# Performance work log

Hardware: AMD Instinct MI355X
Metric: run time of the kernel (lower is better)

The kernel has to match this reference:

```python
import jax, jax.numpy as jnp
import numpy as np
from jax import lax

C = 128
N_HEADS = 4
HEAD_D = C // N_HEADS
EXP = 2  # FFN expansion


def _ln_c(x, g, b, eps):
    # LayerNorm over channel dim of NCHW (equivalent to to_3d -> LN(c) -> to_4d)
    m = jnp.mean(x, axis=1, keepdims=True)
    v = jnp.mean((x - m) ** 2, axis=1, keepdims=True)
    return (x - m) / jnp.sqrt(v + eps) * g[None, :, None, None] + b[None, :, None, None]


def _conv1x1(x, w, b):
    # w: (out, in)
    return jnp.einsum('bchw,oc->bohw', x, w) + b[None, :, None, None]


def _dwconv(x, w, b):
    # depthwise conv, w: (Cg, 1, k, k), stride 1, SAME padding
    y = lax.conv_general_dilated(
        x, w, window_strides=(1, 1), padding='SAME',
        dimension_numbers=('NCHW', 'OIHW', 'NCHW'),
        feature_group_count=x.shape[1])
    return y + b[None, :, None, None]


def setup_inputs() -> dict:
    key = jax.random.key(0)
    ks = jax.random.split(key, 24)
    s = 0.05
    hid = C
    e = EXP * C
    inp = {
        'feats1': jax.random.normal(ks[0], (2, C, 64, 256), jnp.float32),
        'feats2': jax.random.normal(ks[1], (2, C, 64, 256), jnp.float32),
        # attention norms
        'an_g': jnp.ones((C,), jnp.float32), 'an_b': jnp.zeros((C,), jnp.float32),
        'anc_g': jnp.ones((C,), jnp.float32), 'anc_b': jnp.zeros((C,), jnp.float32),
        # qkv / out 1x1 convs
        'wq': jax.random.normal(ks[2], (hid, C), jnp.float32) * s,
        'bq': jnp.zeros((hid,), jnp.float32),
        'wkv': jax.random.normal(ks[3], (2 * hid, C), jnp.float32) * s,
        'bkv': jnp.zeros((2 * hid,), jnp.float32),
        'wo': jax.random.normal(ks[4], (C, hid), jnp.float32) * s,
        'bo': jnp.zeros((C,), jnp.float32),
        # FFN
        'fn_g': jnp.ones((C,), jnp.float32), 'fn_b': jnp.zeros((C,), jnp.float32),
        'w_in': jax.random.normal(ks[5], (e, C), jnp.float32) * s,
        'b_in': jnp.zeros((e,), jnp.float32),
        'w_dw3': jax.random.normal(ks[6], (e, 1, 3, 3), jnp.float32) * s,
        'b_dw3': jnp.zeros((e,), jnp.float32),
        'w_dw5': jax.random.normal(ks[7], (e, 1, 5, 5), jnp.float32) * s,
        'b_dw5': jnp.zeros((e,), jnp.float32),
        'w_dw7': jax.random.normal(ks[8], (e, 1, 7, 7), jnp.float32) * s,
        'b_dw7': jnp.zeros((e,), jnp.float32),
        'w_pw': jax.random.normal(ks[9], (e, 3 * e), jnp.float32) * s,
        'b_pw': jnp.zeros((e,), jnp.float32),
        'w_out': jax.random.normal(ks[10], (C, e), jnp.float32) * s,
        'b_out': jnp.zeros((C,), jnp.float32),
    }
    return inp


def reference(feats1, feats2, an_g, an_b, anc_g, anc_b, wq, bq, wkv, bkv, wo, bo,
              fn_g, fn_b, w_in, b_in, w_dw3, b_dw3, w_dw5, b_dw5, w_dw7, b_dw7,
              w_pw, b_pw, w_out, b_out):
    eps = 1e-6
    hid = C
    n, d = N_HEADS, HEAD_D
    scale = d ** (-0.5)

    # bi-directional cross attention: doubled batch
    cat1 = jnp.concatenate([feats1, feats2], axis=0)  # (B, C, H, W)
    cat2 = jnp.concatenate([feats2, feats1], axis=0)
    B, _, H, W = cat1.shape

    # pre-norm (separate norms for query and context streams)
    x1 = _ln_c(cat1, an_g, an_b, eps)
    x2 = _ln_c(cat2, anc_g, anc_b, eps)

    q = _conv1x1(x1, wq, bq)                     # (B, hid, H, W)
    kv = _conv1x1(x2, wkv, bkv)
    k, v = kv[:, :hid], kv[:, hid:]

    qh = q.reshape(B, n, d, H, W)
    kh = k.reshape(B, n, d, H, W)
    vh = v.reshape(B, n, d, H, W)

    # per-row (epipolar) attention over width
    sim = jnp.einsum('bndhi,bndhj->bnhij', qh, kh) * scale  # (B, n, H, W, W)
    # sink competition renorm
    attn = jax.nn.softmax(sim, axis=-1) + eps
    attn = attn / jnp.sum(attn, axis=-1, keepdims=True)

    o = jnp.einsum('bnhij,bndhj->bndhi', attn, vh).reshape(B, hid, H, W)
    o = _conv1x1(o, wo, bo)
    cat1 = cat1 + o

    # multiscale depthwise-conv FFN (receptive_aug='conv')
    y = _ln_c(cat1, fn_g, fn_b, 1e-5)
    y = jax.nn.silu(_conv1x1(y, w_in, b_in))     # (B, 2C, H, W)
    f3 = _dwconv(y, w_dw3, b_dw3)
    f5 = _dwconv(y, w_dw5, b_dw5)
    f7 = _dwconv(y, w_dw7, b_dw7)
    y = y + jax.nn.silu(_conv1x1(jnp.concatenate([f3, f5, f7], axis=1), w_pw, b_pw))
    y = _conv1x1(y, w_out, b_out)
    cat1 = cat1 + y

    half = B // 2
    return cat1[:half], cat1[half:]
```

## Files before the change

kernel.cpp:

```cpp
#include <hip/hip_runtime.h>

typedef unsigned short u16;
typedef unsigned int u32;

constexpr int H_ = 64;
constexpr int W_ = 256;
constexpr int HW_ = H_ * W_;

typedef __bf16 bf16x8 __attribute__((ext_vector_type(8)));
typedef float f32x4 __attribute__((ext_vector_type(4)));

__device__ __forceinline__ float bf2f(u16 v) { return __uint_as_float(((u32)v) << 16); }
__device__ __forceinline__ u16 f2bf(float f) {
  u32 x = __float_as_uint(f);
  u32 r = (x + 0x7fffu + ((x >> 16) & 1u)) >> 16;
  return (u16)r;
}
__device__ __forceinline__ float lo2f(u32 p) { return __uint_as_float(p << 16); }
__device__ __forceinline__ float hi2f(u32 p) { return __uint_as_float(p & 0xffff0000u); }
__device__ __forceinline__ void unpack8(uint4 v, float* f) {
  f[0] = lo2f(v.x); f[1] = hi2f(v.x);
  f[2] = lo2f(v.y); f[3] = hi2f(v.y);
  f[4] = lo2f(v.z); f[5] = hi2f(v.z);
  f[6] = lo2f(v.w); f[7] = hi2f(v.w);
}
__device__ __forceinline__ bf16x8 as_bf16x8(uint4 v) {
  union { uint4 u; bf16x8 b; } x; x.u = v; return x.b;
}
__device__ __forceinline__ int swz(int p, int c) { return c ^ (((p >> 3) & 3) << 3); }

constexpr int NT = 26;
constexpr int ELEMS_PER_BLK = 4096;
struct CvtArgs {
  const void* src[NT];
  u32 dst_off[NT];
  u32 n[NT];
  u32 blk_start[NT];
};

__global__ void convert_all(CvtArgs a, u16* __restrict__ dst) {
  const u32 bid = blockIdx.x;
  int ti = 0;
#pragma unroll
  for (int k = 1; k < NT; ++k) if (a.blk_start[k] <= bid) ti = k;
  const u32 e0 = (bid - a.blk_start[ti]) * ELEMS_PER_BLK;
  const u32 n = a.n[ti];
  u32 hi = e0 + ELEMS_PER_BLK; if (hi > n) hi = n;
  const float* sp = (const float*)a.src[ti];
  u16* d = dst + a.dst_off[ti];
  for (u32 i = e0 + threadIdx.x; i < hi; i += 256) d[i] = f2bf(sp[i]);
}

template <int CIN, int COUT>
__launch_bounds__(256)
__global__ void gemm1x1_ln(const u16* __restrict__ xA, const u16* __restrict__ xB,
                           const u16* __restrict__ w, const u16* __restrict__ bias,
                           const u16* __restrict__ lng, const u16* __restrict__ lnb,
                           float lneps, u16* __restrict__ out) {
  constexpr int POS = 64;
  constexpr int PITCH = CIN + 8;
  constexpr int MT = COUT / 64;
  __shared__ __align__(16) u16 xs[POS * PITCH];
  __shared__ float red1[256], red2[256], stm[64], str[64];
  const int t = threadIdx.x;
  const int b = blockIdx.y;
  const int pos0 = blockIdx.x * POS;

  const u16* basep = (b >= 2) ? xB : xA;
  const int bb = (b < 2) ? b : b - 2;
  const u16* xb16 = basep + (size_t)bb * CIN * HW_;

  constexpr int NLOAD = CIN * POS / 8;
  for (int idx = t; idx < NLOAD; idx += 256) {
    const int c = idx / (POS / 8);
    const int p8 = (idx % (POS / 8)) * 8;
    uint4 v = *(const uint4*)(xb16 + (size_t)c * HW_ + pos0 + p8);
    const int csw = swz(p8, c);
    u16* row = xs + p8 * PITCH + csw;
    row[0]         = (u16)v.x; row[PITCH]     = (u16)(v.x >> 16);
    row[2 * PITCH] = (u16)v.y; row[3 * PITCH] = (u16)(v.y >> 16);
    row[4 * PITCH] = (u16)v.z; row[5 * PITCH] = (u16)(v.z >> 16);
    row[6 * PITCH] = (u16)v.w; row[7 * PITCH] = (u16)(v.w >> 16);
  }
  __syncthreads();

  {
    const int p = t & 63, part = t >> 6;
    const int xorp = ((p >> 3) & 3) << 3;
    float s = 0.f, sq = 0.f;
#pragma unroll
    for (int k = 0; k < 32; k += 8) {
      uint4 v = *(const uint4*)(xs + p * PITCH + ((part * 32 + k) ^ xorp));
      float f[8]; unpack8(v, f);
#pragma unroll
      for (int j = 0; j < 8; ++j) { s += f[j]; sq += f[j] * f[j]; }
    }
    red1[part * 64 + p] = s; red2[part * 64 + p] = sq;
    __syncthreads();
    if (t < 64) {
      float ss = red1[t] + red1[64 + t] + red1[128 + t] + red1[192 + t];
      float qq = red2[t] + red2[64 + t] + red2[128 + t] + red2[192 + t];
      float m = ss * (1.0f / CIN);
      float var = qq * (1.0f / CIN) - m * m;
      var = var < 0.f ? 0.f : var;
      stm[t] = m; str[t] = rsqrtf(var + lneps);
    }
    __syncthreads();
    const float m = stm[p], r = str[p];
#pragma unroll
    for (int k = 0; k < 32; k += 8) {
      const int c = part * 32 + k;
      uint4 v = *(const uint4*)(xs + p * PITCH + (c ^ xorp));
      float f[8]; unpack8(v, f);
      u32 pk[4];
#pragma unroll
      for (int j = 0; j < 8; j += 2) {
        float g0 = bf2f(lng[c + j]), be0 = bf2f(lnb[c + j]);
        float g1 = bf2f(lng[c + j + 1]), be1 = bf2f(lnb[c + j + 1]);
        u16 lo = f2bf((f[j] - m) * r * g0 + be0);
        u16 hi = f2bf((f[j + 1] - m) * r * g1 + be1);
        pk[j >> 1] = (u32)lo | ((u32)hi << 16);
      }
      uint4 ov; ov.x = pk[0]; ov.y = pk[1]; ov.z = pk[2]; ov.w = pk[3];
      *(uint4*)(xs + p * PITCH + (c ^ xorp)) = ov;
    }
    __syncthreads();
  }

  const int lane = t & 63, wv = t >> 6;
  const int lo16 = lane & 15, quad = lane >> 4;
  const int orow0 = wv * MT * 16;
  const int qrow = quad * 4;

  f32x4 acc[MT][4];
#pragma unroll
  for (int mt = 0; mt < MT; ++mt) {
#pragma unroll
    for (int r = 0; r < 4; ++r) {
      const float bv = bf2f(bias[orow0 + mt * 16 + qrow + r]);
#pragma unroll
      for (int nt = 0; nt < 4; ++nt) acc[mt][nt][r] = bv;
    }
  }

  const u16* xb[4];
#pragma unroll
  for (int nt = 0; nt < 4; ++nt) {
    const int row = nt * 16 + lo16;
    xb[nt] = xs + row * PITCH + (quad * 8 ^ ((((row >> 3) & 3)) << 3));
  }
  const u16* wl = w + (size_t)(orow0 + lo16) * CIN + quad * 8;

#pragma unroll 2
  for (int kc = 0; kc < CIN / 32; ++kc) {
    const int c0 = kc * 32;
    bf16x8 bfr[4];
#pragma unroll
    for (int nt = 0; nt < 4; ++nt)
      bfr[nt] = as_bf16x8(*(const uint4*)(xb[nt] + c0));
#pragma unroll
    for (int mt = 0; mt < MT; ++mt) {
      bf16x8 afr = as_bf16x8(*(const uint4*)(wl + (size_t)mt * 16 * CIN + c0));
#pragma unroll
      for (int nt = 0; nt < 4; ++nt)
        acc[mt][nt] = __builtin_amdgcn_mfma_f32_16x16x32_bf16(afr, bfr[nt], acc[mt][nt], 0, 0, 0);
    }
  }

#pragma unroll
  for (int mt = 0; mt < MT; ++mt) {
#pragma unroll
    for (int nt = 0; nt < 4; ++nt) {
#pragma unroll
      for (int r = 0; r < 4; ++r) {
        const int o = orow0 + mt * 16 + qrow + r;
        const int p = pos0 + nt * 16 + lo16;
        out[((size_t)b * COUT + o) * HW_ + p] = f2bf(acc[mt][nt][r]);
      }
    }
  }
}

__launch_bounds__(256)
__global__ void attn_mfma(const u16* __restrict__ qb, const u16* __restrict__ kvb,
                          u16* __restrict__ ob) {
  constexpr int PA = 40;
  constexpr int PJ = 264;
  __shared__ __align__(16) u16 kT[256 * PA];
  __shared__ __align__(16) u16 vT[32 * PJ];
  __shared__ __align__(16) u16 PlO[4 * 16 * PJ];
  const int t = threadIdx.x;
  const int h = blockIdx.x, n = blockIdx.y, b = blockIdx.z;
  const size_t qbase = ((size_t)(b * 128 + n * 32)) * HW_ + (size_t)h * W_;
  const size_t kbase = ((size_t)(b * 256 + n * 32)) * HW_ + (size_t)h * W_;
  const size_t vbase = ((size_t)(b * 256 + 128 + n * 32)) * HW_ + (size_t)h * W_;

#pragma unroll
  for (int d8 = 0; d8 < 4; ++d8) {
    u32 pk[4];
#pragma unroll
    for (int j = 0; j < 4; ++j) {
      u32 lo = kvb[kbase + (size_t)(d8 * 8 + 2 * j) * HW_ + t];
      u32 hi = kvb[kbase + (size_t)(d8 * 8 + 2 * j + 1) * HW_ + t];
      pk[j] = lo | (hi << 16);
    }
    *(uint4*)(kT + t * PA + d8 * 8) = make_uint4(pk[0], pk[1], pk[2], pk[3]);
  }
#pragma unroll
  for (int k = 0; k < 16; ++k) {
    const int idx = k * 256 + t;
    const int d = idx >> 7, p2 = (idx & 127) * 2;
    u32 v = *(const u32*)(kvb + vbase + (size_t)d * HW_ + p2);
    *(u32*)(vT + d * PJ + p2) = v;
  }
  __syncthreads();

  const int lane = t & 63, wv = t >> 6;
  const int lo16 = lane & 15, quad = lane >> 4;
  const float scale = 0.17677669529663687f;
  const float renorm = 1.0f / (1.0f + 256.0f * 1e-6f);
  const float addc = 1e-6f * renorm;
  u16* Pw = PlO + wv * 16 * PJ;

  f32x4 oacc[4][2];
  for (int ii = 0; ii < 4; ++ii) {
    const int i0 = ii * 64 + wv * 16;
    u16 qr[8];
#pragma unroll
    for (int j = 0; j < 8; ++j)
      qr[j] = qb[qbase + (size_t)(quad * 8 + j) * HW_ + i0 + lo16];
    bf16x8 qa;
#pragma unroll
    for (int j = 0; j < 8; ++j) qa[j] = *(__bf16*)&qr[j];
    f32x4 s[16];
#pragma unroll
    for (int jt = 0; jt < 16; ++jt) {
      bf16x8 kb = as_bf16x8(*(const uint4*)(kT + (jt * 16 + lo16) * PA + quad * 8));
      f32x4 z = {0.f, 0.f, 0.f, 0.f};
      s[jt] = __builtin_amdgcn_mfma_f32_16x16x32_bf16(qa, kb, z, 0, 0, 0);
    }
#pragma unroll
    for (int r = 0; r < 4; ++r) {
      float sum = 0.f;
#pragma unroll
      for (int jt = 0; jt < 16; ++jt) {
        float e = __expf(s[jt][r] * scale);
        s[jt][r] = e; sum += e;
      }
#pragma unroll
      for (int off = 1; off <= 8; off <<= 1) sum += __shfl_xor(sum, off, 64);
      const float inv2 = renorm / sum;
#pragma unroll
      for (int jt = 0; jt < 16; ++jt)
        Pw[(quad * 4 + r) * PJ + jt * 16 + lo16] = f2bf(fmaf(s[jt][r], inv2, addc));
    }
    f32x4 o0 = {0.f, 0.f, 0.f, 0.f}, o1 = {0.f, 0.f, 0.f, 0.f};
#pragma unroll
    for (int kt = 0; kt < 8; ++kt) {
      bf16x8 pa = as_bf16x8(*(const uint4*)(Pw + lo16 * PJ + kt * 32 + quad * 8));
      bf16x8 v0 = as_bf16x8(*(const uint4*)(vT + lo16 * PJ + kt * 32 + quad * 8));
      bf16x8 v1 = as_bf16x8(*(const uint4*)(vT + (16 + lo16) * PJ + kt * 32 + quad * 8));
      o0 = __builtin_amdgcn_mfma_f32_16x16x32_bf16(pa, v0, o0, 0, 0, 0);
      o1 = __builtin_amdgcn_mfma_f32_16x16x32_bf16(pa, v1, o1, 0, 0, 0);
    }
    oacc[ii][0] = o0; oacc[ii][1] = o1;
  }
  __syncthreads();
  u16* Ob = PlO;
#pragma unroll
  for (int ii = 0; ii < 4; ++ii) {
    const int i0 = ii * 64 + wv * 16;
#pragma unroll
    for (int r = 0; r < 4; ++r) {
      Ob[(i0 + quad * 4 + r) * PA + lo16] = f2bf(oacc[ii][0][r]);
      Ob[(i0 + quad * 4 + r) * PA + 16 + lo16] = f2bf(oacc[ii][1][r]);
    }
  }
  __syncthreads();
  for (int d = 0; d < 32; ++d) ob[qbase + (size_t)d * HW_ + t] = Ob[t * PA + d];
}

__launch_bounds__(256)
__global__ void fused_proj_ffn(const u16* __restrict__ obf,
                               const u16* __restrict__ wo, const u16* __restrict__ bo_,
                               const float* __restrict__ f1, const float* __restrict__ f2,
                               const u16* __restrict__ fng, const u16* __restrict__ fnb,
                               const u16* __restrict__ w_in, const u16* __restrict__ b_in,
                               u16* __restrict__ cat1b, u16* __restrict__ yb) {
  constexpr int PITCH = 136;
  __shared__ __align__(16) u16 xs[64 * PITCH];
  __shared__ float red1[256], red2[256], stm[64], str[64];
  const int t = threadIdx.x;
  const int b = blockIdx.y;
  const int pos0 = blockIdx.x * 64;
  const u16* xb16 = obf + (size_t)b * 128 * HW_;

  for (int idx = t; idx < 1024; idx += 256) {
    const int c = idx >> 3, p8 = (idx & 7) * 8;
    uint4 v = *(const uint4*)(xb16 + (size_t)c * HW_ + pos0 + p8);
    const int csw = swz(p8, c);
    u16* row = xs + p8 * PITCH + csw;
    row[0]         = (u16)v.x; row[PITCH]     = (u16)(v.x >> 16);
    row[2 * PITCH] = (u16)v.y; row[3 * PITCH] = (u16)(v.y >> 16);
    row[4 * PITCH] = (u16)v.z; row[5 * PITCH] = (u16)(v.z >> 16);
    row[6 * PITCH] = (u16)v.w; row[7 * PITCH] = (u16)(v.w >> 16);
  }
  __syncthreads();

  const int lane = t & 63, wv = t >> 6;
  const int lo16 = lane & 15, quad = lane >> 4, qrow = quad * 4;
  const u16* xb[4];
#pragma unroll
  for (int nt = 0; nt < 4; ++nt) {
    const int row = nt * 16 + lo16;
    xb[nt] = xs + row * PITCH + (quad * 8 ^ ((((row >> 3) & 3)) << 3));
  }

  const int orow0 = wv * 32;
  f32x4 acc1[2][4];
#pragma unroll
  for (int mt = 0; mt < 2; ++mt)
#pragma unroll
    for (int r = 0; r < 4; ++r) {
      const float bv = bf2f(bo_[orow0 + mt * 16 + qrow + r]);
#pragma unroll
      for (int nt = 0; nt < 4; ++nt) acc1[mt][nt][r] = bv;
    }
  const u16* wl1 = wo + (size_t)(orow0 + lo16) * 128 + quad * 8;
#pragma unroll
  for (int kc = 0; kc < 4; ++kc) {
    const int c0 = kc * 32;
    bf16x8 bfr[4];
#pragma unroll
    for (int nt = 0; nt < 4; ++nt) bfr[nt] = as_bf16x8(*(const uint4*)(xb[nt] + c0));
#pragma unroll
    for (int mt = 0; mt < 2; ++mt) {
      bf16x8 afr = as_bf16x8(*(const uint4*)(wl1 + (size_t)mt * 16 * 128 + c0));
#pragma unroll
      for (int nt = 0; nt < 4; ++nt)
        acc1[mt][nt] = __builtin_amdgcn_mfma_f32_16x16x32_bf16(afr, bfr[nt], acc1[mt][nt], 0, 0, 0);
    }
  }
  __syncthreads();

  {
    const int bl = (b < 2) ? b : b - 2;
    const float* rb = (b < 2) ? f1 : f2;
#pragma unroll
    for (int mt = 0; mt < 2; ++mt)
#pragma unroll
      for (int nt = 0; nt < 4; ++nt)
#pragma unroll
        for (int r = 0; r < 4; ++r) {
          const int o = orow0 + mt * 16 + qrow + r;
          const int p = nt * 16 + lo16;
          float v = acc1[mt][nt][r] + rb[((size_t)bl * 128 + o) * HW_ + pos0 + p];
          const u16 bv = f2bf(v);
          cat1b[((size_t)b * 128 + o) * HW_ + pos0 + p] = bv;
          xs[p * PITCH + swz(p, o)] = bv;
        }
  }
  __syncthreads();

  {
    const int p = t & 63, part = t >> 6;
    const int xorp = ((p >> 3) & 3) << 3;
    float s = 0.f, sq = 0.f;
#pragma unroll
    for (int k = 0; k < 32; k += 8) {
      uint4 v = *(const uint4*)(xs + p * PITCH + ((part * 32 + k) ^ xorp));
      float f[8]; unpack8(v, f);
#pragma unroll
      for (int j = 0; j < 8; ++j) { s += f[j]; sq += f[j] * f[j]; }
    }
    red1[part * 64 + p] = s; red2[part * 64 + p] = sq;
    __syncthreads();
    if (t < 64) {
      float ss = red1[t] + red1[64 + t] + red1[128 + t] + red1[192 + t];
      float qq = red2[t] + red2[64 + t] + red2[128 + t] + red2[192 + t];
      float m = ss * (1.0f / 128.0f);
      float var = qq * (1.0f / 128.0f) - m * m;
      var = var < 0.f ? 0.f : var;
      stm[t] = m; str[t] = rsqrtf(var + 1e-5f);
    }
    __syncthreads();
    const float m = stm[p], r = str[p];
#pragma unroll
    for (int k = 0; k < 32; k += 8) {
      const int c = part * 32 + k;
      uint4 v = *(const uint4*)(xs + p * PITCH + (c ^ xorp));
      float f[8]; unpack8(v, f);
      u32 pk[4];
#pragma unroll
      for (int j = 0; j < 8; j += 2) {
        float g0 = bf2f(fng[c + j]), be0 = bf2f(fnb[c + j]);
        float g1 = bf2f(fng[c + j + 1]), be1 = bf2f(fnb[c + j + 1]);
        u16 lo = f2bf((f[j] - m) * r * g0 + be0);
        u16 hi = f2bf((f[j + 1] - m) * r * g1 + be1);
        pk[j >> 1] = (u32)lo | ((u32)hi << 16);
      }
      uint4 ov; ov.x = pk[0]; ov.y = pk[1]; ov.z = pk[2]; ov.w = pk[3];
      *(uint4*)(xs + p * PITCH + (c ^ xorp)) = ov;
    }
    __syncthreads();
  }

  const int orow2 = wv * 64;
  f32x4 acc2[4][4];
#pragma unroll
  for (int mt = 0; mt < 4; ++mt)
#pragma unroll
    for (int r = 0; r < 4; ++r) {
      const float bv = bf2f(b_in[orow2 + mt * 16 + qrow + r]);
#pragma unroll
      for (int nt = 0; nt < 4; ++nt) acc2[mt][nt][r] = bv;
    }
  const u16* wl2 = w_in + (size_t)(orow2 + lo16) * 128 + quad * 8;
#pragma unroll
  for (int kc = 0; kc < 4; ++kc) {
    const int c0 = kc * 32;
    bf16x8 bfr[4];
#pragma unroll
    for (int nt = 0; nt < 4; ++nt) bfr[nt] = as_bf16x8(*(const uint4*)(xb[nt] + c0));
#pragma unroll
    for (int mt = 0; mt < 4; ++mt) {
      bf16x8 afr = as_bf16x8(*(const uint4*)(wl2 + (size_t)mt * 16 * 128 + c0));
#pragma unroll
      for (int nt = 0; nt < 4; ++nt)
        acc2[mt][nt] = __builtin_amdgcn_mfma_f32_16x16x32_bf16(afr, bfr[nt], acc2[mt][nt], 0, 0, 0);
    }
  }
#pragma unroll
  for (int mt = 0; mt < 4; ++mt)
#pragma unroll
    for (int nt = 0; nt < 4; ++nt)
#pragma unroll
      for (int r = 0; r < 4; ++r) {
        const int o = orow2 + mt * 16 + qrow + r;
        const int p = nt * 16 + lo16;
        float v = acc2[mt][nt][r];
        v = v / (1.0f + __expf(-v));
        yb[((size_t)b * 256 + o) * HW_ + pos0 + p] = f2bf(v);
      }
}

__launch_bounds__(256)
__global__ void fused_pw_out(const u16* __restrict__ fbase, size_t f_stride,
                             const u16* __restrict__ w_pw, const u16* __restrict__ b_pw,
                             const u16* __restrict__ yb,
                             const u16* __restrict__ w_out, const u16* __restrict__ b_out,
                             const u16* __restrict__ cat1b, float* __restrict__ outp,
                             int b_off) {
  constexpr int P1 = 776, P2 = 264;
  __shared__ __align__(16) u16 buf[64 * P1];
  const int t = threadIdx.x;
  const int bo2 = (int)blockIdx.y + b_off;
  const int pos0 = blockIdx.x * 64;
  const u16* xf = fbase + (size_t)blockIdx.y * f_stride;

  for (int idx = t; idx < 6144; idx += 256) {
    const int c = idx >> 3, p8 = (idx & 7) * 8;
    uint4 v = *(const uint4*)(xf + (size_t)c * HW_ + pos0 + p8);
    const int csw = swz(p8, c);
    u16* row = buf + p8 * P1 + csw;
    row[0]      = (u16)v.x; row[P1]     = (u16)(v.x >> 16);
    row[2 * P1] = (u16)v.y; row[3 * P1] = (u16)(v.y >> 16);
    row[4 * P1] = (u16)v.z; row[5 * P1] = (u16)(v.z >> 16);
    row[6 * P1] = (u16)v.w; row[7 * P1] = (u16)(v.w >> 16);
  }
  __syncthreads();

  const int lane = t & 63, wv = t >> 6;
  const int lo16 = lane & 15, quad = lane >> 4, qrow = quad * 4;

  const u16* xb1[4];
#pragma unroll
  for (int nt = 0; nt < 4; ++nt) {
    const int row = nt * 16 + lo16;
    xb1[nt] = buf + row * P1 + (quad * 8 ^ ((((row >> 3) & 3)) << 3));
  }
  const int orow1 = wv * 64;
  f32x4 acc[4][4];
#pragma unroll
  for (int mt = 0; mt < 4; ++mt)
#pragma unroll
    for (int r = 0; r < 4; ++r) {
      const float bv = bf2f(b_pw[orow1 + mt * 16 + qrow + r]);
#pragma unroll
      for (int nt = 0; nt < 4; ++nt) acc[mt][nt][r] = bv;
    }
  const u16* wl1 = w_pw + (size_t)(orow1 + lo16) * 768 + quad * 8;
#pragma unroll 2
  for (int kc = 0; kc < 24; ++kc) {
    const int c0 = kc * 32;
    bf16x8 bfr[4];
#pragma unroll
    for (int nt = 0; nt < 4; ++nt) bfr[nt] = as_bf16x8(*(const uint4*)(xb1[nt] + c0));
#pragma unroll
    for (int mt = 0; mt < 4; ++mt) {
      bf16x8 afr = as_bf16x8(*(const uint4*)(wl1 + (size_t)mt * 16 * 768 + c0));
#pragma unroll
      for (int nt = 0; nt < 4; ++nt)
        acc[mt][nt] = __builtin_amdgcn_mfma_f32_16x16x32_bf16(afr, bfr[nt], acc[mt][nt], 0, 0, 0);
    }
  }
  __syncthreads();

#pragma unroll
  for (int mt = 0; mt < 4; ++mt)
#pragma unroll
    for (int nt = 0; nt < 4; ++nt)
#pragma unroll
      for (int r = 0; r < 4; ++r) {
        const int o = orow1 + mt * 16 + qrow + r;
        const int p = nt * 16 + lo16;
        float v = acc[mt][nt][r];
        v = v / (1.0f + __expf(-v));
        v += bf2f(yb[((size_t)bo2 * 256 + o) * HW_ + pos0 + p]);
        buf[p * P2 + swz(p, o)] = f2bf(v);
      }
  __syncthreads();

  const u16* xb2[4];
#pragma unroll
  for (int nt = 0; nt < 4; ++nt) {
    const int row = nt * 16 + lo16;
    xb2[nt] = buf + row * P2 + (quad * 8 ^ ((((row >> 3) & 3)) << 3));
  }
  const int orow2 = wv * 32;
  f32x4 acc2[2][4];
#pragma unroll
  for (int mt = 0; mt < 2; ++mt)
#pragma unroll
    for (int r = 0; r < 4; ++r) {
      const float bv = bf2f(b_out[orow2 + mt * 16 + qrow + r]);
#pragma unroll
      for (int nt = 0; nt < 4; ++nt) acc2[mt][nt][r] = bv;
    }
  const u16* wl2 = w_out + (size_t)(orow2 + lo16) * 256 + quad * 8;
#pragma unroll
  for (int kc = 0; kc < 8; ++kc) {
    const int c0 = kc * 32;
    bf16x8 bfr[4];
#pragma unroll
    for (int nt = 0; nt < 4; ++nt) bfr[nt] = as_bf16x8(*(const uint4*)(xb2[nt] + c0));
#pragma unroll
    for (int mt = 0; mt < 2; ++mt) {
      bf16x8 afr = as_bf16x8(*(const uint4*)(wl2 + (size_t)mt * 16 * 256 + c0));
#pragma unroll
      for (int nt = 0; nt < 4; ++nt)
        acc2[mt][nt] = __builtin_amdgcn_mfma_f32_16x16x32_bf16(afr, bfr[nt], acc2[mt][nt], 0, 0, 0);
    }
  }
#pragma unroll
  for (int mt = 0; mt < 2; ++mt)
#pragma unroll
    for (int nt = 0; nt < 4; ++nt)
#pragma unroll
      for (int r = 0; r < 4; ++r) {
        const int o = orow2 + mt * 16 + qrow + r;
        const int p = nt * 16 + lo16;
        const size_t gidx = ((size_t)bo2 * 128 + o) * HW_ + pos0 + p;
        outp[gidx] = acc2[mt][nt][r] + bf2f(cat1b[gidx]);
      }
}

__launch_bounds__(256)
__global__ void dwconv_kernel(const u16* __restrict__ yB,
                              const u16* __restrict__ w3, const u16* __restrict__ b3,
                              const u16* __restrict__ w5, const u16* __restrict__ b5,
                              const u16* __restrict__ w7, const u16* __restrict__ b7,
                              u16* __restrict__ fB) {
  constexpr int LW = 70, LH = 14, LP = 72;
  __shared__ u16 tile[LH * LP];
  __shared__ float wf7[49], wf5[25], wf3[9];
  const int t = threadIdx.x;
  const int c = blockIdx.y;
  const int bz = blockIdx.z;
  const int tw = blockIdx.x & 3, th = blockIdx.x >> 2;
  const int w0 = tw * 64, h0 = th * 8;
  const u16* src = yB + ((size_t)bz * 256 + c) * HW_;

  if (t < 49) wf7[t] = bf2f(w7[c * 49 + t]);
  if (t >= 64 && t < 89) wf5[t - 64] = bf2f(w5[c * 25 + (t - 64)]);
  if (t >= 96 && t < 105) wf3[t - 96] = bf2f(w3[c * 9 + (t - 96)]);

  for (int idx = t; idx < LH * LW; idx += 256) {
    const int r = idx / LW, cc = idx - r * LW;
    const int gh = h0 + r - 3, gw = w0 + cc - 3;
    u16 v = 0;
    if (gh >= 0 && gh < H_ && gw >= 0 && gw < W_) v = src[gh * W_ + gw];
    tile[r * LP + cc] = v;
  }
  __syncthreads();

  const int x0 = (t & 31) * 2;
  const int hh = t >> 5;
  float a3x = 0.f, a3y = 0.f, a5x = 0.f, a5y = 0.f, a7x = 0.f, a7y = 0.f;
#pragma unroll
  for (int rr = 0; rr < 7; ++rr) {
    const u16* trow = tile + (hh + rr) * LP + x0;
    float f[10];
#pragma unroll
    for (int k = 0; k < 5; ++k) {
      u32 v = *(const u32*)(trow + 2 * k);
      f[2 * k] = lo2f(v); f[2 * k + 1] = hi2f(v);
    }
#pragma unroll
    for (int dx = 0; dx < 7; ++dx) {
      const float wv = wf7[rr * 7 + dx];
      a7x += wv * f[dx]; a7y += wv * f[dx + 1];
    }
    if (rr >= 1 && rr <= 5) {
#pragma unroll
      for (int dx = 0; dx < 5; ++dx) {
        const float wv = wf5[(rr - 1) * 5 + dx];
        a5x += wv * f[dx + 1]; a5y += wv * f[dx + 2];
      }
    }
    if (rr >= 2 && rr <= 4) {
#pragma unroll
      for (int dx = 0; dx < 3; ++dx) {
        const float wv = wf3[(rr - 2) * 3 + dx];
        a3x += wv * f[dx + 2]; a3y += wv * f[dx + 3];
      }
    }
  }
  const float B3v = bf2f(b3[c]), B5v = bf2f(b5[c]), B7v = bf2f(b7[c]);
  const size_t o0 = (size_t)bz * 768 * HW_ + (size_t)c * HW_ + (size_t)(h0 + hh) * W_ + (w0 + x0);
  *(u32*)(fB + o0) = (u32)f2bf(a3x + B3v) | ((u32)f2bf(a3y + B3v) << 16);
  *(u32*)(fB + o0 + (size_t)256 * HW_) = (u32)f2bf(a5x + B5v) | ((u32)f2bf(a5y + B5v) << 16);
  *(u32*)(fB + o0 + (size_t)512 * HW_) = (u32)f2bf(a7x + B7v) | ((u32)f2bf(a7y + B7v) << 16);
}

extern "C" void kernel_launch(void* const* d_in, const int* in_sizes, int n_in,
                              void* d_out, int out_size, void* d_ws, size_t ws_size,
                              hipStream_t stream) {
  (void)out_size; (void)n_in;
  char* ws = (char*)d_ws;
  const size_t MB = 1ull << 20;

  u16* arena = (u16*)ws;
  CvtArgs ca;
  u32 off = 0, blk = 0;
  u32 aoff[NT];
  for (int i = 0; i < NT; ++i) {
    ca.src[i] = d_in[i];
    ca.n[i] = (u32)in_sizes[i];
    ca.dst_off[i] = off;
    aoff[i] = off;
    ca.blk_start[i] = blk;
    off += (ca.n[i] + 15u) & ~15u;
    blk += (ca.n[i] + ELEMS_PER_BLK - 1) / ELEMS_PER_BLK;
  }
  const u32 total_blocks = blk;

  const u16* f1c   = arena + aoff[0];
  const u16* f2c   = arena + aoff[1];
  const u16* an_g  = arena + aoff[2];
  const u16* an_b  = arena + aoff[3];
  const u16* anc_g = arena + aoff[4];
  const u16* anc_b = arena + aoff[5];
  const u16* wq    = arena + aoff[6];
  const u16* bq    = arena + aoff[7];
  const u16* wkv   = arena + aoff[8];
  const u16* bkv   = arena + aoff[9];
  const u16* wo    = arena + aoff[10];
  const u16* bo_   = arena + aoff[11];
  const u16* fn_g  = arena + aoff[12];
  const u16* fn_b  = arena + aoff[13];
  const u16* w_in  = arena + aoff[14];
  const u16* b_in  = arena + aoff[15];
  const u16* w3    = arena + aoff[16];
  const u16* b3    = arena + aoff[17];
  const u16* w5    = arena + aoff[18];
  const u16* b5    = arena + aoff[19];
  const u16* w7    = arena + aoff[20];
  const u16* b7    = arena + aoff[21];
  const u16* w_pw  = arena + aoff[22];
  const u16* b_pw  = arena + aoff[23];
  const u16* w_out = arena + aoff[24];
  const u16* b_out = arena + aoff[25];

  u16* cat1b  = (u16*)(ws + 18 * MB);
  u16* qb     = (u16*)(ws + 34 * MB);
  u16* kvb    = (u16*)(ws + 50 * MB);
  u16* obf    = (u16*)(ws + 82 * MB);
  u16* yb     = (u16*)(ws + 34 * MB);
  u16* fbuf   = (u16*)(ws + 66 * MB);
  float* outp = (float*)d_out;
  const bool big = ws_size >= 168 * MB;

  dim3 blk256(256);
  convert_all<<<total_blocks, 256, 0, stream>>>(ca, arena);

  gemm1x1_ln<128, 128><<<dim3(HW_ / 64, 4), blk256, 0, stream>>>(
      f1c, f2c, wq, bq, an_g, an_b, 1e-6f, qb);
  gemm1x1_ln<128, 256><<<dim3(HW_ / 64, 4), blk256, 0, stream>>>(
      f2c, f1c, wkv, bkv, anc_g, anc_b, 1e-6f, kvb);
  attn_mfma<<<dim3(64, 4, 4), blk256, 0, stream>>>(qb, kvb, obf);
  fused_proj_ffn<<<dim3(HW_ / 64, 4), blk256, 0, stream>>>(
      obf, wo, bo_, (const float*)d_in[0], (const float*)d_in[1],
      fn_g, fn_b, w_in, b_in, cat1b, yb);
  if (big) {
    dwconv_kernel<<<dim3(32, 256, 4), blk256, 0, stream>>>(yb, w3, b3, w5, b5, w7, b7, fbuf);
    fused_pw_out<<<dim3(HW_ / 64, 4), blk256, 0, stream>>>(
        fbuf, (size_t)768 * HW_, w_pw, b_pw, yb, w_out, b_out, cat1b, outp, 0);
  } else {
    for (int b = 0; b < 4; ++b) {
      dwconv_kernel<<<dim3(32, 256, 1), blk256, 0, stream>>>(
          yb + (size_t)b * 256 * HW_, w3, b3, w5, b5, w7, b7, fbuf);
      fused_pw_out<<<dim3(HW_ / 64, 1), blk256, 0, stream>>>(
          fbuf, 0, w_pw, b_pw, yb, w_out, b_out, cat1b, outp, b);
    }
  }
}
```

Before: 436.2 us.

## Double-buffer channel chunks in fused_pw_out with 512-thread blocks

The fused pointwise-plus-output kernel no longer stages all 768 input channels in a 99KB LDS tile. It streams 128-channel chunks through a double-buffered 34KB LDS tile, prefetching the next chunk from global memory into registers while MFMAs consume the current one. The block grows to 512 threads (8 waves), so each wave owns fewer output rows and the accumulator register footprint halves. This is meant to raise occupancy and overlap global loads with compute, at the cost of more barriers per block.

```diff
diff --git a/kernel.cpp b/kernel.cpp
--- a/kernel.cpp
+++ b/kernel.cpp
@@ -444,70 +444,110 @@
       }
 }
 
-__launch_bounds__(256)
+__launch_bounds__(512, 4)
 __global__ void fused_pw_out(const u16* __restrict__ fbase, size_t f_stride,
                              const u16* __restrict__ w_pw, const u16* __restrict__ b_pw,
                              const u16* __restrict__ yb,
                              const u16* __restrict__ w_out, const u16* __restrict__ b_out,
                              const u16* __restrict__ cat1b, float* __restrict__ outp,
                              int b_off) {
-  constexpr int P1 = 776, P2 = 264;
-  __shared__ __align__(16) u16 buf[64 * P1];
+  constexpr int SP = 136;
+  constexpr int P2 = 264;
+  constexpr int NCHK = 6;
+  __shared__ __align__(16) u16 sbuf[2][64 * SP];
+  u16* y2 = &sbuf[0][0];
+
   const int t = threadIdx.x;
   const int bo2 = (int)blockIdx.y + b_off;
   const int pos0 = blockIdx.x * 64;
   const u16* xf = fbase + (size_t)blockIdx.y * f_stride;
 
-  for (int idx = t; idx < 6144; idx += 256) {
-    const int c = idx >> 3, p8 = (idx & 7) * 8;
-    uint4 v = *(const uint4*)(xf + (size_t)c * HW_ + pos0 + p8);
-    const int csw = swz(p8, c);
-    u16* row = buf + p8 * P1 + csw;
-    row[0]      = (u16)v.x; row[P1]     = (u16)(v.x >> 16);
-    row[2 * P1] = (u16)v.y; row[3 * P1] = (u16)(v.y >> 16);
-    row[4 * P1] = (u16)v.z; row[5 * P1] = (u16)(v.z >> 16);
-    row[6 * P1] = (u16)v.w; row[7 * P1] = (u16)(v.w >> 16);
-  }
-  __syncthreads();
-
   const int lane = t & 63, wv = t >> 6;
   const int lo16 = lane & 15, quad = lane >> 4, qrow = quad * 4;
 
-  const u16* xb1[4];
+  const int c_s0 = t >> 3;
+  const int c_s1 = c_s0 + 64;
+  const int p8_s = (t & 7) * 8;
+  const size_t g_off = pos0 + p8_s;
+
+  uint4 pf0, pf1;
+  pf0 = *(const uint4*)(xf + (size_t)c_s0 * HW_ + g_off);
+  pf1 = *(const uint4*)(xf + (size_t)c_s1 * HW_ + g_off);
+  {
+    u16* r0 = sbuf[0] + p8_s * SP + swz(p8_s, c_s0);
+    r0[0]      = (u16)pf0.x; r0[SP]     = (u16)(pf0.x >> 16);
+    r0[2 * SP] = (u16)pf0.y; r0[3 * SP] = (u16)(pf0.y >> 16);
+    r0[4 * SP] = (u16)pf0.z; r0[5 * SP] = (u16)(pf0.z >> 16);
+    r0[6 * SP] = (u16)pf0.w; r0[7 * SP] = (u16)(pf0.w >> 16);
+    u16* r1 = sbuf[0] + p8_s * SP + swz(p8_s, c_s1);
+    r1[0]      = (u16)pf1.x; r1[SP]     = (u16)(pf1.x >> 16);
+    r1[2 * SP] = (u16)pf1.y; r1[3 * SP] = (u16)(pf1.y >> 16);
+    r1[4 * SP] = (u16)pf1.z; r1[5 * SP] = (u16)(pf1.z >> 16);
+    r1[6 * SP] = (u16)pf1.w; r1[7 * SP] = (u16)(pf1.w >> 16);
+  }
+  pf0 = *(const uint4*)(xf + (size_t)(128 + c_s0) * HW_ + g_off);
+  pf1 = *(const uint4*)(xf + (size_t)(128 + c_s1) * HW_ + g_off);
+
+  const int orow1 = wv * 32;
+  f32x4 acc[2][4];
+#pragma unroll
+  for (int mt = 0; mt < 2; ++mt)
+#pragma unroll
+    for (int r = 0; r < 4; ++r) {
+      const float bv = bf2f(b_pw[orow1 + mt * 16 + qrow + r]);
+#pragma unroll
+      for (int nt = 0; nt < 4; ++nt) acc[mt][nt][r] = bv;
+    }
+  int xoff[4];
 #pragma unroll
   for (int nt = 0; nt < 4; ++nt) {
     const int row = nt * 16 + lo16;
-    xb1[nt] = buf + row * P1 + (quad * 8 ^ ((((row >> 3) & 3)) << 3));
-  }
-  const int orow1 = wv * 64;
-  f32x4 acc[4][4];
-#pragma unroll
-  for (int mt = 0; mt < 4; ++mt)
-#pragma unroll
-    for (int r = 0; r < 4; ++r) {
-      const float bv = bf2f(b_pw[orow1 + mt * 16 + qrow + r]);
-#pragma unroll
-      for (int nt = 0; nt < 4; ++nt) acc[mt][nt][r] = bv;
-    }
+    xoff[nt] = row * SP + (quad * 8 ^ ((((row >> 3) & 3)) << 3));
+  }
   const u16* wl1 = w_pw + (size_t)(orow1 + lo16) * 768 + quad * 8;
-#pragma unroll 2
-  for (int kc = 0; kc < 24; ++kc) {
-    const int c0 = kc * 32;
-    bf16x8 bfr[4];
-#pragma unroll
-    for (int nt = 0; nt < 4; ++nt) bfr[nt] = as_bf16x8(*(const uint4*)(xb1[nt] + c0));
-#pragma unroll
-    for (int mt = 0; mt < 4; ++mt) {
-      bf16x8 afr = as_bf16x8(*(const uint4*)(wl1 + (size_t)mt * 16 * 768 + c0));
+
+  __syncthreads();
+
+  for (int ch = 0; ch < NCHK; ++ch) {
+    if (ch + 1 < NCHK) {
+      u16* dst = sbuf[(ch + 1) & 1];
+      u16* r0 = dst + p8_s * SP + swz(p8_s, c_s0);
+      r0[0]      = (u16)pf0.x; r0[SP]     = (u16)(pf0.x >> 16);
+      r0[2 * SP] = (u16)pf0.y; r0[3 * SP] = (u16)(pf0.y >> 16);
+      r0[4 * SP] = (u16)pf0.z; r0[5 * SP] = (u16)(pf0.z >> 16);
+      r0[6 * SP] = (u16)pf0.w; r0[7 * SP] = (u16)(pf0.w >> 16);
+      u16* r1 = dst + p8_s * SP + swz(p8_s, c_s1);
+      r1[0]      = (u16)pf1.x; r1[SP]     = (u16)(pf1.x >> 16);
+      r1[2 * SP] = (u16)pf1.y; r1[3 * SP] = (u16)(pf1.y >> 16);
+      r1[4 * SP] = (u16)pf1.z; r1[5 * SP] = (u16)(pf1.z >> 16);
+      r1[6 * SP] = (u16)pf1.w; r1[7 * SP] = (u16)(pf1.w >> 16);
+    }
+    if (ch + 2 < NCHK) {
+      pf0 = *(const uint4*)(xf + (size_t)((ch + 2) * 128 + c_s0) * HW_ + g_off);
+      pf1 = *(const uint4*)(xf + (size_t)((ch + 2) * 128 + c_s1) * HW_ + g_off);
+    }
+    const u16* xs = sbuf[ch & 1];
+    const u16* wch = wl1 + ch * 128;
+#pragma unroll
+    for (int kc = 0; kc < 4; ++kc) {
+      const int c0 = kc * 32;
+      bf16x8 bfr[4];
 #pragma unroll
       for (int nt = 0; nt < 4; ++nt)
-        acc[mt][nt] = __builtin_amdgcn_mfma_f32_16x16x32_bf16(afr, bfr[nt], acc[mt][nt], 0, 0, 0);
-    }
-  }
-  __syncthreads();
-
-#pragma unroll
-  for (int mt = 0; mt < 4; ++mt)
+        bfr[nt] = as_bf16x8(*(const uint4*)(xs + xoff[nt] + c0));
+#pragma unroll
+      for (int mt = 0; mt < 2; ++mt) {
+        bf16x8 afr = as_bf16x8(*(const uint4*)(wch + (size_t)mt * 16 * 768 + c0));
+#pragma unroll
+        for (int nt = 0; nt < 4; ++nt)
+          acc[mt][nt] = __builtin_amdgcn_mfma_f32_16x16x32_bf16(afr, bfr[nt], acc[mt][nt], 0, 0, 0);
+      }
+    }
+    __syncthreads();
+  }
+
+#pragma unroll
+  for (int mt = 0; mt < 2; ++mt)
 #pragma unroll
     for (int nt = 0; nt < 4; ++nt)
 #pragma unroll
@@ -517,52 +557,45 @@
         float v = acc[mt][nt][r];
         v = v / (1.0f + __expf(-v));
         v += bf2f(yb[((size_t)bo2 * 256 + o) * HW_ + pos0 + p]);
-        buf[p * P2 + swz(p, o)] = f2bf(v);
-      }
-  __syncthreads();
-
-  const u16* xb2[4];
+        y2[p * P2 + swz(p, o)] = f2bf(v);
+      }
+  __syncthreads();
+
+  int x2off[4];
 #pragma unroll
   for (int nt = 0; nt < 4; ++nt) {
     const int row = nt * 16 + lo16;
-    xb2[nt] = buf + row * P2 + (quad * 8 ^ ((((row >> 3) & 3)) << 3));
-  }
-  const int orow2 = wv * 32;
-  f32x4 acc2[2][4];
-#pragma unroll
-  for (int mt = 0; mt < 2; ++mt)
-#pragma unroll
-    for (int r = 0; r < 4; ++r) {
-      const float bv = bf2f(b_out[orow2 + mt * 16 + qrow + r]);
-#pragma unroll
-      for (int nt = 0; nt < 4; ++nt) acc2[mt][nt][r] = bv;
-    }
+    x2off[nt] = row * P2 + (quad * 8 ^ ((((row >> 3) & 3)) << 3));
+  }
+  const int orow2 = wv * 16;
+  f32x4 acc2[4];
+#pragma unroll
+  for (int r = 0; r < 4; ++r) {
+    const float bv = bf2f(b_out[orow2 + qrow + r]);
+#pragma unroll
+    for (int nt = 0; nt < 4; ++nt) acc2[nt][r] = bv;
+  }
   const u16* wl2 = w_out + (size_t)(orow2 + lo16) * 256 + quad * 8;
 #pragma unroll
   for (int kc = 0; kc < 8; ++kc) {
     const int c0 = kc * 32;
     bf16x8 bfr[4];
 #pragma unroll
-    for (int nt = 0; nt < 4; ++nt) bfr[nt] = as_bf16x8(*(const uint4*)(xb2[nt] + c0));
-#pragma unroll
-    for (int mt = 0; mt < 2; ++mt) {
-      bf16x8 afr = as_bf16x8(*(const uint4*)(wl2 + (size_t)mt * 16 * 256 + c0));
-#pragma unroll
-      for (int nt = 0; nt < 4; ++nt)
-        acc2[mt][nt] = __builtin_amdgcn_mfma_f32_16x16x32_bf16(afr, bfr[nt], acc2[mt][nt], 0, 0, 0);
-    }
-  }
-#pragma unroll
-  for (int mt = 0; mt < 2; ++mt)
+    for (int nt = 0; nt < 4; ++nt) bfr[nt] = as_bf16x8(*(const uint4*)(y2 + x2off[nt] + c0));
+    bf16x8 afr = as_bf16x8(*(const uint4*)(wl2 + c0));
 #pragma unroll
     for (int nt = 0; nt < 4; ++nt)
-#pragma unroll
-      for (int r = 0; r < 4; ++r) {
-        const int o = orow2 + mt * 16 + qrow + r;
-        const int p = nt * 16 + lo16;
-        const size_t gidx = ((size_t)bo2 * 128 + o) * HW_ + pos0 + p;
-        outp[gidx] = acc2[mt][nt][r] + bf2f(cat1b[gidx]);
-      }
+      acc2[nt] = __builtin_amdgcn_mfma_f32_16x16x32_bf16(afr, bfr[nt], acc2[nt], 0, 0, 0);
+  }
+#pragma unroll
+  for (int nt = 0; nt < 4; ++nt)
+#pragma unroll
+    for (int r = 0; r < 4; ++r) {
+      const int o = orow2 + qrow + r;
+      const int p = nt * 16 + lo16;
+      const size_t gidx = ((size_t)bo2 * 128 + o) * HW_ + pos0 + p;
+      outp[gidx] = acc2[nt][r] + bf2f(cat1b[gidx]);
+    }
 }
 
 __launch_bounds__(256)
@@ -692,6 +725,7 @@
   const bool big = ws_size >= 168 * MB;
 
   dim3 blk256(256);
+  dim3 blk512(512);
   convert_all<<<total_blocks, 256, 0, stream>>>(ca, arena);
 
   gemm1x1_ln<128, 128><<<dim3(HW_ / 64, 4), blk256, 0, stream>>>(
@@ -704,13 +738,13 @@
       fn_g, fn_b, w_in, b_in, cat1b, yb);
   if (big) {
     dwconv_kernel<<<dim3(32, 256, 4), blk256, 0, stream>>>(yb, w3, b3, w5, b5, w7, b7, fbuf);
-    fused_pw_out<<<dim3(HW_ / 64, 4), blk256, 0, stream>>>(
+    fused_pw_out<<<dim3(HW_ / 64, 4), blk512, 0, stream>>>(
         fbuf, (size_t)768 * HW_, w_pw, b_pw, yb, w_out, b_out, cat1b, outp, 0);
   } else {
     for (int b = 0; b < 4; ++b) {
       dwconv_kernel<<<dim3(32, 256, 1), blk256, 0, stream>>>(
           yb + (size_t)b * 256 * HW_, w3, b3, w5, b5, w7, b7, fbuf);
-      fused_pw_out<<<dim3(HW_ / 64, 1), blk256, 0, stream>>>(
+      fused_pw_out<<<dim3(HW_ / 64, 1), blk512, 0, stream>>>(
           fbuf, 0, w_pw, b_pw, yb, w_out, b_out, cat1b, outp, b);
     }
   }
```

After: 376.9 us. 13.6% less time.
